# Optimization experiments

Measured on AMD Instinct MI355X. Metric: run time of the kernel, lower is better.

## Reference

```python
import jax, jax.numpy as jnp
import numpy as np

N, IN_DIM, HID, H = 4096, 128, 512, 8
D = HID // H  # head_dim = 64
NEG = -1e9


def setup_inputs() -> dict:
    key = jax.random.key(0)
    ks = jax.random.split(key, 16)
    s_in = 1.0 / np.sqrt(IN_DIM)
    s_h = 1.0 / np.sqrt(HID)
    return {
        "node_features": jax.random.normal(ks[0], (N, IN_DIM), jnp.float32),
        "edge_mask_bool": jax.random.bernoulli(ks[1], 0.3, (1, 1, N, N)),
        "time_bias": jax.random.normal(ks[2], (1, 1, N, N), jnp.float32) * 0.1,
        "W_in": jax.random.normal(ks[3], (IN_DIM, HID), jnp.float32) * s_in,
        "b_in": jnp.zeros((HID,), jnp.float32),
        "Wq": jax.random.normal(ks[4], (HID, HID), jnp.float32) * s_h,
        "bq": jnp.zeros((HID,), jnp.float32),
        "Wk": jax.random.normal(ks[5], (HID, HID), jnp.float32) * s_h,
        "bk": jnp.zeros((HID,), jnp.float32),
        "Wv": jax.random.normal(ks[6], (HID, HID), jnp.float32) * s_h,
        "bv": jnp.zeros((HID,), jnp.float32),
        "Wo": jax.random.normal(ks[7], (HID, HID), jnp.float32) * s_h,
        "bo": jnp.zeros((HID,), jnp.float32),
    }


def reference(node_features, edge_mask_bool, time_bias, W_in, b_in, Wq, bq, Wk, bk, Wv, bv, Wo, bo):
    # input projection + QKV projections
    x = node_features @ W_in + b_in                       # [N, HID]
    q = (x @ Wq + bq).reshape(N, H, D)                    # [N, H, D]
    k = (x @ Wk + bk).reshape(N, H, D)
    v = (x @ Wv + bv).reshape(N, H, D)
    # scores [H, N, N], scaled by sqrt(head_dim)
    scores = jnp.einsum("nhd,mhd->hnm", q, k) / jnp.sqrt(jnp.asarray(D, x.dtype))
    # additive mask: True blocks attention (-1e9), plus time bias
    bias = edge_mask_bool[0, 0].astype(x.dtype) * NEG + time_bias[0, 0]  # [N, N]
    scores = scores + bias[None, :, :]
    attn = jax.nn.softmax(scores, axis=-1)                # [H, N, N]
    out = jnp.einsum("hnm,mhd->nhd", attn, v).reshape(N, HID)
    return out @ Wo + bo                                  # [N, HID]
```

## Files before the change

### kernel.cpp

```cpp
#include <hip/hip_runtime.h>
#include <hip/hip_bf16.h>

static constexpr int kN   = 4096;
static constexpr int kIn  = 128;
static constexpr int kHid = 512;
static constexpr int kH   = 8;
static constexpr int kD   = 64;
#define NEGV (-1e9f)

static constexpr int kKFS = 32768 + 64;
static constexpr int kVFS = 131072 + 64;

typedef __bf16 bf16x8 __attribute__((ext_vector_type(8)));
typedef float  f32x4  __attribute__((ext_vector_type(4)));
typedef float  f32x16 __attribute__((ext_vector_type(16)));

__device__ __forceinline__ unsigned short f2bf(float f) {
    return __builtin_bit_cast(unsigned short, (__bf16)f);
}
__device__ __forceinline__ unsigned pkbf(float a, float b) {
    return (unsigned)f2bf(a) | ((unsigned)f2bf(b) << 16);
}

__global__ void misc_kernel(const unsigned int* __restrict__ m, int* __restrict__ mode,
                            const float* __restrict__ bq, const float* __restrict__ bk,
                            const float* __restrict__ bv, float* __restrict__ dst) {
    if (blockIdx.x < 6) {
        int i = blockIdx.x * 256 + threadIdx.x;
        dst[i] = i < 512 ? bq[i] : (i < 1024 ? bk[i - 512] : bv[i - 1024]);
        return;
    }
    int t = threadIdx.x;
    if (t >= 64) return;
    int isf = 0, isb = 0;
    for (int i = t; i < 4096; i += 64) {
        unsigned int w = m[i];
        if (w == 0x3F800000u) isf = 1;
        else if (w > 1u)      isb = 1;
    }
    unsigned long long bf = __ballot(isf != 0);
    unsigned long long bb = __ballot(isb != 0);
    if (t == 0) mode[0] = bf ? 2 : (bb ? 1 : 0);
}

__global__ void transpose_all_kernel(const float* __restrict__ s0, const float* __restrict__ s1,
                                     const float* __restrict__ s2, const float* __restrict__ s3,
                                     const float* __restrict__ s4,
                                     unsigned short* __restrict__ d0, unsigned short* __restrict__ d1,
                                     unsigned short* __restrict__ d2, unsigned short* __restrict__ d3,
                                     unsigned short* __restrict__ d4) {
    __shared__ float t[32][33];
    int z = blockIdx.z;
    const float* src = z == 0 ? s0 : z == 1 ? s1 : z == 2 ? s2 : z == 3 ? s3 : s4;
    unsigned short* dst = z == 0 ? d0 : z == 1 ? d1 : z == 2 ? d2 : z == 3 ? d3 : d4;
    int R = z == 0 ? kIn : kHid, C = kHid;
    int c0 = blockIdx.x * 32, r0 = blockIdx.y * 32;
    if (r0 >= R) return;
    int tx = threadIdx.x, ty = threadIdx.y;
#pragma unroll
    for (int i = 0; i < 4; i++) {
        int r = ty + i * 8;
        t[r][tx] = src[(size_t)(r0 + r) * C + c0 + tx];
    }
    __syncthreads();
#pragma unroll
    for (int i = 0; i < 4; i++) {
        int r = ty + i * 8;
        dst[(size_t)(c0 + r) * R + r0 + tx] = f2bf(t[tx][r]);
    }
}

template <bool ABF, int OMODE>
__global__ __launch_bounds__(256) void gemm_kernel(const void* __restrict__ Ap,
                                                   const unsigned short* __restrict__ Bt,
                                                   const float* __restrict__ bias,
                                                   void* __restrict__ Cp, void* __restrict__ Cp2,
                                                   void* __restrict__ Cp3,
                                                   int M, int Nn, int K, int ldc) {
    __shared__ unsigned short As[128][40];
    __shared__ unsigned short Bs[128][40];
    const int tid  = threadIdx.x;
    const int lane = tid & 63;
    const int wv   = tid >> 6;
    const int wr   = wv >> 1, wc = wv & 1;
    const int m0 = blockIdx.x * 128, n0 = blockIdx.y * 128;
    const int g = lane >> 4, li = lane & 15;

    f32x4 acc[4][4] = {};
    const int rr = tid >> 2;
    const int cc = (tid & 3) * 8;

    for (int k0 = 0; k0 < K; k0 += 32) {
#pragma unroll
        for (int p = 0; p < 128; p += 64) {
            int r = rr + p;
            if (ABF) {
                const unsigned short* A = (const unsigned short*)Ap;
                *(uint4*)&As[r][cc] = *(const uint4*)(A + (size_t)(m0 + r) * K + k0 + cc);
            } else {
                const float* A = (const float*)Ap;
                const float4 v0 = *(const float4*)(A + (size_t)(m0 + r) * K + k0 + cc);
                const float4 v1 = *(const float4*)(A + (size_t)(m0 + r) * K + k0 + cc + 4);
                uint4 u;
                u.x = f2bf(v0.x) | ((unsigned)f2bf(v0.y) << 16);
                u.y = f2bf(v0.z) | ((unsigned)f2bf(v0.w) << 16);
                u.z = f2bf(v1.x) | ((unsigned)f2bf(v1.y) << 16);
                u.w = f2bf(v1.z) | ((unsigned)f2bf(v1.w) << 16);
                *(uint4*)&As[r][cc] = u;
            }
            *(uint4*)&Bs[r][cc] = *(const uint4*)(Bt + (size_t)(n0 + r) * K + k0 + cc);
        }
        __syncthreads();

        bf16x8 af[4], bfv[4];
#pragma unroll
        for (int mi = 0; mi < 4; mi++)
            af[mi] = *(const bf16x8*)&As[wr * 64 + mi * 16 + li][g * 8];
#pragma unroll
        for (int ni = 0; ni < 4; ni++)
            bfv[ni] = *(const bf16x8*)&Bs[wc * 64 + ni * 16 + li][g * 8];
#pragma unroll
        for (int mi = 0; mi < 4; mi++)
#pragma unroll
            for (int ni = 0; ni < 4; ni++)
                acc[mi][ni] = __builtin_amdgcn_mfma_f32_16x16x32_bf16(af[mi], bfv[ni], acc[mi][ni], 0, 0, 0);
        __syncthreads();
    }

#pragma unroll
    for (int mi = 0; mi < 4; mi++) {
        int rowb = m0 + wr * 64 + mi * 16 + g * 4;
#pragma unroll
        for (int ni = 0; ni < 4; ni++) {
            int col = n0 + wc * 64 + ni * 16 + li;
            float bv = bias ? bias[col] : 0.f;
            if (OMODE == 3) {
                if (col < 512) {
                    unsigned short* C = (unsigned short*)Cp;
#pragma unroll
                    for (int r2 = 0; r2 < 4; r2++)
                        C[(size_t)(rowb + r2) * 512 + col] = f2bf(acc[mi][ni][r2] + bv);
                } else if (col < 1024) {
                    int d = col - 512;
                    unsigned short* Kf = (unsigned short*)Cp2;
                    size_t base = (size_t)(d >> 3) * kKFS + (size_t)(d & 7);
#pragma unroll
                    for (int r2 = 0; r2 < 4; r2++)
                        Kf[base + ((size_t)(rowb + r2) << 3)] = f2bf(acc[mi][ni][r2] + bv);
                } else {
                    int d = col - 1024;
                    unsigned short* Vf = (unsigned short*)Cp3;
                    size_t base = (size_t)(d >> 5) * kVFS + ((size_t)(rowb >> 3) << 8) +
                                  ((size_t)(d & 31) << 3) + (size_t)(rowb & 7);
                    ushort4 st;
                    st.x = f2bf(acc[mi][ni][0] + bv);
                    st.y = f2bf(acc[mi][ni][1] + bv);
                    st.z = f2bf(acc[mi][ni][2] + bv);
                    st.w = f2bf(acc[mi][ni][3] + bv);
                    *(ushort4*)(Vf + base) = st;
                }
            } else if (OMODE == 1) {
                unsigned short* C = (unsigned short*)Cp;
#pragma unroll
                for (int r2 = 0; r2 < 4; r2++)
                    C[(size_t)(rowb + r2) * ldc + col] = f2bf(acc[mi][ni][r2] + bv);
            } else {
                float* C = (float*)Cp;
#pragma unroll
                for (int r2 = 0; r2 < 4; r2++)
                    C[(size_t)(rowb + r2) * ldc + col] = acc[mi][ni][r2] + bv;
            }
        }
    }
}

__global__ __launch_bounds__(512, 4) void attn_kernel(
    const unsigned short* __restrict__ qg, const unsigned short* __restrict__ kfb,
    const unsigned short* __restrict__ vfb,
    const void* __restrict__ maskp, const float* __restrict__ tb,
    const int* __restrict__ modep,
    float* __restrict__ Op, float* __restrict__ Mp, float* __restrict__ Lp,
    int KZ, int NC) {
    __shared__ float bias_s[2][128][33];

    const int tid  = threadIdx.x;
    const int lane = tid & 63;
    const int w    = tid >> 6;
    const int q5   = lane & 31;
    const int hi   = lane >> 5;
    const int n0   = blockIdx.x * 32;
    const int z    = blockIdx.y;
    const int kz0  = z * KZ;
    const int mode = modep[0];
    const int hb   = w * kD;

    bf16x8 qf[4];
#pragma unroll
    for (int f = 0; f < 4; f++)
        qf[f] = *(const bf16x8*)(qg + (size_t)(n0 + q5) * 512 + hb + f * 16 + hi * 8);

    f32x16 po[2] = {};
    float m_run = -3e38f, l_run = 0.f;

    const int sr  = tid & 31;
    const int scg = tid >> 5;
    float stg[8];

    auto stage_load = [&](int kbase) {
        size_t idx = (size_t)(n0 + sr) * kN + kbase + scg * 8;
        float tv[8];
        *(float4*)&tv[0] = *(const float4*)(tb + idx);
        *(float4*)&tv[4] = *(const float4*)(tb + idx + 4);
        if (mode == 0) {
            const int* mp = (const int*)maskp;
            int4 a = *(const int4*)(mp + idx);
            int4 b = *(const int4*)(mp + idx + 4);
            int mv[8] = {a.x, a.y, a.z, a.w, b.x, b.y, b.z, b.w};
#pragma unroll
            for (int j = 0; j < 8; j++) stg[j] = (mv[j] ? NEGV : 0.f) + tv[j];
        } else if (mode == 1) {
            const unsigned char* mp = (const unsigned char*)maskp;
            uint2 u = *(const uint2*)(mp + idx);
#pragma unroll
            for (int j = 0; j < 4; j++) stg[j] = (((u.x >> (8 * j)) & 255u) ? NEGV : 0.f) + tv[j];
#pragma unroll
            for (int j = 0; j < 4; j++) stg[4 + j] = (((u.y >> (8 * j)) & 255u) ? NEGV : 0.f) + tv[4 + j];
        } else {
            const float* mp = (const float*)maskp;
            float4 a = *(const float4*)(mp + idx);
            float4 b = *(const float4*)(mp + idx + 4);
            float mv[8] = {a.x, a.y, a.z, a.w, b.x, b.y, b.z, b.w};
#pragma unroll
            for (int j = 0; j < 8; j++) stg[j] = (mv[j] != 0.f ? NEGV : 0.f) + tv[j];
        }
    };
    auto stage_write = [&](int buf) {
#pragma unroll
        for (int j = 0; j < 8; j++) bias_s[buf][scg * 8 + j][sr] = stg[j];
    };

    auto kload = [&](int kpos, int f) -> bf16x8 {
        return *(const bf16x8*)(kfb + (size_t)(w * 8 + f * 2 + hi) * kKFS + ((size_t)(kpos + q5) << 3));
    };

    stage_load(kz0);
    stage_write(0);
    __syncthreads();

    for (int c = 0; c < NC; c++) {
        if (c + 1 < NC) stage_load(kz0 + (c + 1) * 128);
        const int cb = c & 1;
        const int kbase = kz0 + c * 128;

        bf16x8 kcur[4], knxt[4];
#pragma unroll
        for (int f = 0; f < 4; f++) kcur[f] = kload(kbase, f);

#pragma unroll
        for (int s = 0; s < 4; s++) {
            const int kpos = kbase + s * 32;
            bf16x8 vb00, vb01, vb10, vb11;
            {
                const size_t v0 = (size_t)(w * 2 + 0) * kVFS + (((size_t)kpos >> 3) << 8) + ((size_t)q5 << 3);
                const size_t v1 = (size_t)(w * 2 + 1) * kVFS + (((size_t)kpos >> 3) << 8) + ((size_t)q5 << 3);
                vb00 = *(const bf16x8*)(vfb + v0 + ((size_t)hi << 8));
                vb01 = *(const bf16x8*)(vfb + v0 + ((size_t)(2 + hi) << 8));
                vb10 = *(const bf16x8*)(vfb + v1 + ((size_t)hi << 8));
                vb11 = *(const bf16x8*)(vfb + v1 + ((size_t)(2 + hi) << 8));
            }
            if (s < 3) {
#pragma unroll
                for (int f = 0; f < 4; f++) knxt[f] = kload(kbase + (s + 1) * 32, f);
            }
            f32x16 sc = {};
#pragma unroll
            for (int f = 0; f < 4; f++)
                sc = __builtin_amdgcn_mfma_f32_32x32x16_bf16(kcur[f], qf[f], sc, 0, 0, 0);

            float v[16];
#pragma unroll
            for (int r = 0; r < 16; r++) {
                int key = (r & 3) + 8 * (r >> 2) + 4 * hi;
                v[r] = fmaf(sc[r], 0.125f, bias_s[cb][s * 32 + key][q5]);
            }
            float t8[8];
#pragma unroll
            for (int i = 0; i < 8; i++) t8[i] = fmaxf(v[2 * i], v[2 * i + 1]);
#pragma unroll
            for (int i = 0; i < 4; i++) t8[i] = fmaxf(t8[i], t8[i + 4]);
            t8[0] = fmaxf(t8[0], t8[2]); t8[1] = fmaxf(t8[1], t8[3]);
            float mx = fmaxf(t8[0], t8[1]);
            mx = fmaxf(mx, __shfl_xor(mx, 32));
            if (!__all(mx <= m_run + 8.0f)) {
                float mnew = fmaxf(m_run, mx);
                float alpha = __expf(m_run - mnew);
                m_run = mnew;
                l_run *= alpha;
                po[0] *= alpha;
                po[1] *= alpha;
            }
            float p[16], s8[8];
#pragma unroll
            for (int i = 0; i < 8; i++) {
                p[2 * i]     = __expf(v[2 * i] - m_run);
                p[2 * i + 1] = __expf(v[2 * i + 1] - m_run);
                s8[i] = p[2 * i] + p[2 * i + 1];
            }
#pragma unroll
            for (int i = 0; i < 4; i++) s8[i] += s8[i + 4];
            l_run += (s8[0] + s8[2]) + (s8[1] + s8[3]);
            unsigned su[8], tu[8];
#pragma unroll
            for (int i = 0; i < 8; i++) su[i] = pkbf(p[2 * i], p[2 * i + 1]);
#pragma unroll
            for (int i = 0; i < 8; i++) tu[i] = __shfl_xor(su[i], 32);
            uint4 f0 = hi ? uint4{tu[2], tu[3], su[2], su[3]} : uint4{su[0], su[1], tu[0], tu[1]};
            uint4 f1 = hi ? uint4{tu[6], tu[7], su[6], su[7]} : uint4{su[4], su[5], tu[4], tu[5]};
            bf16x8 pf0 = __builtin_bit_cast(bf16x8, f0);
            bf16x8 pf1 = __builtin_bit_cast(bf16x8, f1);
            po[0] = __builtin_amdgcn_mfma_f32_32x32x16_bf16(vb00, pf0, po[0], 0, 0, 0);
            po[0] = __builtin_amdgcn_mfma_f32_32x32x16_bf16(vb01, pf1, po[0], 0, 0, 0);
            po[1] = __builtin_amdgcn_mfma_f32_32x32x16_bf16(vb10, pf0, po[1], 0, 0, 0);
            po[1] = __builtin_amdgcn_mfma_f32_32x32x16_bf16(vb11, pf1, po[1], 0, 0, 0);
            if (s < 3) {
#pragma unroll
                for (int f = 0; f < 4; f++) kcur[f] = knxt[f];
            }
        }
        if (c + 1 < NC) {
            __syncthreads();
            stage_write((c + 1) & 1);
            __syncthreads();
        }
    }

    l_run += __shfl_xor(l_run, 32);
    float* ob = Op + ((((size_t)z * kN + n0 + q5) * kH + w) << 6);
#pragma unroll
    for (int a = 0; a < 2; a++)
#pragma unroll
        for (int m = 0; m < 4; m++) {
            float4 st = {po[a][4 * m], po[a][4 * m + 1], po[a][4 * m + 2], po[a][4 * m + 3]};
            *(float4*)(ob + a * 32 + 8 * m + 4 * hi) = st;
        }
    if (lane < 32) {
        Mp[((size_t)z * kN + n0 + q5) * kH + w] = m_run;
        Lp[((size_t)z * kN + n0 + q5) * kH + w] = l_run;
    }
}

__global__ __launch_bounds__(256) void combine_kernel(const float* __restrict__ Op,
                                                      const float* __restrict__ Mp,
                                                      const float* __restrict__ Lp,
                                                      unsigned short* __restrict__ xo, int NZ) {
    int idx = blockIdx.x * 256 + threadIdx.x;
    int n = idx >> 9, c = idx & 511;
    int h = c >> 6, d = c & 63;
    float m = -3e38f;
    for (int zz = 0; zz < NZ; zz++)
        m = fmaxf(m, Mp[((size_t)zz * kN + n) * kH + h]);
    float num = 0.f, den = 0.f;
    for (int zz = 0; zz < NZ; zz++) {
        float a = __expf(Mp[((size_t)zz * kN + n) * kH + h] - m);
        den += a * Lp[((size_t)zz * kN + n) * kH + h];
        num += a * Op[(((size_t)zz * kN + n) * kH + h) * kD + d];
    }
    xo[idx] = f2bf(num / den);
}

extern "C" void kernel_launch(void* const* d_in, const int* in_sizes, int n_in,
                              void* d_out, int out_size, void* d_ws, size_t ws_size,
                              hipStream_t stream) {
    const float* node = (const float*)d_in[0];
    const void*  mask = d_in[1];
    const float* tb   = (const float*)d_in[2];
    const float* W_in = (const float*)d_in[3];
    const float* b_in = (const float*)d_in[4];
    const float* Wq   = (const float*)d_in[5];
    const float* bq   = (const float*)d_in[6];
    const float* Wk   = (const float*)d_in[7];
    const float* bk   = (const float*)d_in[8];
    const float* Wv   = (const float*)d_in[9];
    const float* bv   = (const float*)d_in[10];
    const float* Wo   = (const float*)d_in[11];
    const float* bo   = (const float*)d_in[12];
    (void)in_sizes; (void)n_in; (void)out_size;

    char* ws = (char*)d_ws;
    size_t off = 0;
    auto alloc = [&](size_t bytes) {
        void* p = ws + off;
        off += (bytes + 255) & ~(size_t)255;
        return p;
    };
    unsigned short* x    = (unsigned short*)alloc((size_t)kN * kHid * 2);
    unsigned short* qb   = (unsigned short*)alloc((size_t)kN * kHid * 2);
    unsigned short* kf   = (unsigned short*)alloc((size_t)64 * kKFS * 2);
    unsigned short* vf   = (unsigned short*)alloc((size_t)16 * kVFS * 2);
    unsigned short* Wt_in  = (unsigned short*)alloc((size_t)kHid * kIn * 2);
    unsigned short* Wt_qkv = (unsigned short*)alloc((size_t)3 * kHid * kHid * 2);
    unsigned short* Wt_o   = (unsigned short*)alloc((size_t)kHid * kHid * 2);
    float* bqkv = (float*)alloc(1536 * 4);
    int*   mode = (int*)alloc(256);
    unsigned short* xo = x;

    size_t fixed = off;
    size_t perz = (((size_t)kN * kHid * 4 + 255) & ~(size_t)255) +
                  2 * (((size_t)kN * kH * 4 + 255) & ~(size_t)255);
    int NZ = 4;
    if (fixed + 4 * perz > ws_size) NZ = 2;
    if (fixed + 2 * perz > ws_size) NZ = 1;
    float* Op = (float*)alloc((size_t)NZ * kN * kHid * 4);
    float* Mp = (float*)alloc((size_t)NZ * kN * kH * 4);
    float* Lp = (float*)alloc((size_t)NZ * kN * kH * 4);

    misc_kernel<<<7, 256, 0, stream>>>((const unsigned int*)mask, mode, bq, bk, bv, bqkv);
    transpose_all_kernel<<<dim3(16, 16, 5), dim3(32, 8), 0, stream>>>(
        W_in, Wq, Wk, Wv, Wo, Wt_in, Wt_qkv, Wt_qkv + (size_t)kHid * kHid,
        Wt_qkv + (size_t)2 * kHid * kHid, Wt_o);

    gemm_kernel<false, 1><<<dim3(kN / 128, kHid / 128), 256, 0, stream>>>(
        node, Wt_in, b_in, x, nullptr, nullptr, kN, kHid, kIn, kHid);
    gemm_kernel<true, 3><<<dim3(kN / 128, 1536 / 128), 256, 0, stream>>>(
        x, Wt_qkv, bqkv, qb, kf, vf, kN, 1536, kHid, 512);

    const int KZ = kN / NZ;
    attn_kernel<<<dim3(kN / 32, NZ), 512, 0, stream>>>(
        qb, kf, vf, mask, tb, mode, Op, Mp, Lp, KZ, KZ / 128);
    combine_kernel<<<(kN * kHid) / 256, 256, 0, stream>>>(Op, Mp, Lp, xo, NZ);

    gemm_kernel<true, 0><<<dim3(kN / 128, kHid / 128), 256, 0, stream>>>(
        xo, Wt_o, bo, d_out, nullptr, nullptr, kN, kHid, kHid, kHid);
}
```

Before: 186.3 us.

## Flatten attention chunk loop and raise wave priority around MFMA blocks

Merges the outer 128-key chunk loop and the inner 4-step loop into one flat loop over 32-key tiles. K fragments are now prefetched across chunk boundaries instead of being reloaded cold at the start of each chunk. It also wraps the QK and PV MFMA groups in s_setprio(1)/s_setprio(0) so waves issuing matrix ops get scheduling priority. The flat loop is no longer fully unrolled over s, so the index math and branch conditions become runtime values, which may cost some extra scalar work.

```diff
diff --git a/kernel.cpp b/kernel.cpp
--- a/kernel.cpp
+++ b/kernel.cpp
@@ -247,89 +247,91 @@
     stage_write(0);
     __syncthreads();
 
-    for (int c = 0; c < NC; c++) {
-        if (c + 1 < NC) stage_load(kz0 + (c + 1) * 128);
-        const int cb = c & 1;
-        const int kbase = kz0 + c * 128;
-
-        bf16x8 kcur[4], knxt[4];
-#pragma unroll
-        for (int f = 0; f < 4; f++) kcur[f] = kload(kbase, f);
-
-#pragma unroll
-        for (int s = 0; s < 4; s++) {
-            const int kpos = kbase + s * 32;
-            bf16x8 vb00, vb01, vb10, vb11;
-            {
-                const size_t v0 = (size_t)(w * 2 + 0) * kVFS + (((size_t)kpos >> 3) << 8) + ((size_t)q5 << 3);
-                const size_t v1 = (size_t)(w * 2 + 1) * kVFS + (((size_t)kpos >> 3) << 8) + ((size_t)q5 << 3);
-                vb00 = *(const bf16x8*)(vfb + v0 + ((size_t)hi << 8));
-                vb01 = *(const bf16x8*)(vfb + v0 + ((size_t)(2 + hi) << 8));
-                vb10 = *(const bf16x8*)(vfb + v1 + ((size_t)hi << 8));
-                vb11 = *(const bf16x8*)(vfb + v1 + ((size_t)(2 + hi) << 8));
-            }
-            if (s < 3) {
-#pragma unroll
-                for (int f = 0; f < 4; f++) knxt[f] = kload(kbase + (s + 1) * 32, f);
-            }
-            f32x16 sc = {};
-#pragma unroll
-            for (int f = 0; f < 4; f++)
-                sc = __builtin_amdgcn_mfma_f32_32x32x16_bf16(kcur[f], qf[f], sc, 0, 0, 0);
-
-            float v[16];
-#pragma unroll
-            for (int r = 0; r < 16; r++) {
-                int key = (r & 3) + 8 * (r >> 2) + 4 * hi;
-                v[r] = fmaf(sc[r], 0.125f, bias_s[cb][s * 32 + key][q5]);
-            }
-            float t8[8];
-#pragma unroll
-            for (int i = 0; i < 8; i++) t8[i] = fmaxf(v[2 * i], v[2 * i + 1]);
-#pragma unroll
-            for (int i = 0; i < 4; i++) t8[i] = fmaxf(t8[i], t8[i + 4]);
-            t8[0] = fmaxf(t8[0], t8[2]); t8[1] = fmaxf(t8[1], t8[3]);
-            float mx = fmaxf(t8[0], t8[1]);
-            mx = fmaxf(mx, __shfl_xor(mx, 32));
-            if (!__all(mx <= m_run + 8.0f)) {
-                float mnew = fmaxf(m_run, mx);
-                float alpha = __expf(m_run - mnew);
-                m_run = mnew;
-                l_run *= alpha;
-                po[0] *= alpha;
-                po[1] *= alpha;
-            }
-            float p[16], s8[8];
-#pragma unroll
-            for (int i = 0; i < 8; i++) {
-                p[2 * i]     = __expf(v[2 * i] - m_run);
-                p[2 * i + 1] = __expf(v[2 * i + 1] - m_run);
-                s8[i] = p[2 * i] + p[2 * i + 1];
-            }
-#pragma unroll
-            for (int i = 0; i < 4; i++) s8[i] += s8[i + 4];
-            l_run += (s8[0] + s8[2]) + (s8[1] + s8[3]);
-            unsigned su[8], tu[8];
-#pragma unroll
-            for (int i = 0; i < 8; i++) su[i] = pkbf(p[2 * i], p[2 * i + 1]);
-#pragma unroll
-            for (int i = 0; i < 8; i++) tu[i] = __shfl_xor(su[i], 32);
-            uint4 f0 = hi ? uint4{tu[2], tu[3], su[2], su[3]} : uint4{su[0], su[1], tu[0], tu[1]};
-            uint4 f1 = hi ? uint4{tu[6], tu[7], su[6], su[7]} : uint4{su[4], su[5], tu[4], tu[5]};
-            bf16x8 pf0 = __builtin_bit_cast(bf16x8, f0);
-            bf16x8 pf1 = __builtin_bit_cast(bf16x8, f1);
-            po[0] = __builtin_amdgcn_mfma_f32_32x32x16_bf16(vb00, pf0, po[0], 0, 0, 0);
-            po[0] = __builtin_amdgcn_mfma_f32_32x32x16_bf16(vb01, pf1, po[0], 0, 0, 0);
-            po[1] = __builtin_amdgcn_mfma_f32_32x32x16_bf16(vb10, pf0, po[1], 0, 0, 0);
-            po[1] = __builtin_amdgcn_mfma_f32_32x32x16_bf16(vb11, pf1, po[1], 0, 0, 0);
-            if (s < 3) {
-#pragma unroll
-                for (int f = 0; f < 4; f++) kcur[f] = knxt[f];
-            }
-        }
-        if (c + 1 < NC) {
+    const int NT = NC * 4;
+    bf16x8 kcur[4], knxt[4];
+#pragma unroll
+    for (int f = 0; f < 4; f++) kcur[f] = kload(kz0, f);
+
+    for (int t = 0; t < NT; t++) {
+        const int kpos = kz0 + t * 32;
+        const int cb = (t >> 2) & 1;
+        const int s = t & 3;
+        if (s == 0 && t + 4 < NT) stage_load(kz0 + (t + 4) * 32);
+
+        bf16x8 vb00, vb01, vb10, vb11;
+        {
+            const size_t v0 = (size_t)(w * 2 + 0) * kVFS + (((size_t)kpos >> 3) << 8) + ((size_t)q5 << 3);
+            const size_t v1 = (size_t)(w * 2 + 1) * kVFS + (((size_t)kpos >> 3) << 8) + ((size_t)q5 << 3);
+            vb00 = *(const bf16x8*)(vfb + v0 + ((size_t)hi << 8));
+            vb01 = *(const bf16x8*)(vfb + v0 + ((size_t)(2 + hi) << 8));
+            vb10 = *(const bf16x8*)(vfb + v1 + ((size_t)hi << 8));
+            vb11 = *(const bf16x8*)(vfb + v1 + ((size_t)(2 + hi) << 8));
+        }
+        if (t + 1 < NT) {
+#pragma unroll
+            for (int f = 0; f < 4; f++) knxt[f] = kload(kz0 + (t + 1) * 32, f);
+        }
+        __builtin_amdgcn_s_setprio(1);
+        f32x16 sc = {};
+#pragma unroll
+        for (int f = 0; f < 4; f++)
+            sc = __builtin_amdgcn_mfma_f32_32x32x16_bf16(kcur[f], qf[f], sc, 0, 0, 0);
+        __builtin_amdgcn_s_setprio(0);
+
+        float v[16];
+#pragma unroll
+        for (int r = 0; r < 16; r++) {
+            int key = (r & 3) + 8 * (r >> 2) + 4 * hi;
+            v[r] = fmaf(sc[r], 0.125f, bias_s[cb][s * 32 + key][q5]);
+        }
+        float t8[8];
+#pragma unroll
+        for (int i = 0; i < 8; i++) t8[i] = fmaxf(v[2 * i], v[2 * i + 1]);
+#pragma unroll
+        for (int i = 0; i < 4; i++) t8[i] = fmaxf(t8[i], t8[i + 4]);
+        t8[0] = fmaxf(t8[0], t8[2]); t8[1] = fmaxf(t8[1], t8[3]);
+        float mx = fmaxf(t8[0], t8[1]);
+        mx = fmaxf(mx, __shfl_xor(mx, 32));
+        if (!__all(mx <= m_run + 8.0f)) {
+            float mnew = fmaxf(m_run, mx);
+            float alpha = __expf(m_run - mnew);
+            m_run = mnew;
+            l_run *= alpha;
+            po[0] *= alpha;
+            po[1] *= alpha;
+        }
+        float p[16], s8[8];
+#pragma unroll
+        for (int i = 0; i < 8; i++) {
+            p[2 * i]     = __expf(v[2 * i] - m_run);
+            p[2 * i + 1] = __expf(v[2 * i + 1] - m_run);
+            s8[i] = p[2 * i] + p[2 * i + 1];
+        }
+#pragma unroll
+        for (int i = 0; i < 4; i++) s8[i] += s8[i + 4];
+        l_run += (s8[0] + s8[2]) + (s8[1] + s8[3]);
+        unsigned su[8], tu[8];
+#pragma unroll
+        for (int i = 0; i < 8; i++) su[i] = pkbf(p[2 * i], p[2 * i + 1]);
+#pragma unroll
+        for (int i = 0; i < 8; i++) tu[i] = __shfl_xor(su[i], 32);
+        uint4 f0 = hi ? uint4{tu[2], tu[3], su[2], su[3]} : uint4{su[0], su[1], tu[0], tu[1]};
+        uint4 f1 = hi ? uint4{tu[6], tu[7], su[6], su[7]} : uint4{su[4], su[5], tu[4], tu[5]};
+        bf16x8 pf0 = __builtin_bit_cast(bf16x8, f0);
+        bf16x8 pf1 = __builtin_bit_cast(bf16x8, f1);
+        __builtin_amdgcn_s_setprio(1);
+        po[0] = __builtin_amdgcn_mfma_f32_32x32x16_bf16(vb00, pf0, po[0], 0, 0, 0);
+        po[0] = __builtin_amdgcn_mfma_f32_32x32x16_bf16(vb01, pf1, po[0], 0, 0, 0);
+        po[1] = __builtin_amdgcn_mfma_f32_32x32x16_bf16(vb10, pf0, po[1], 0, 0, 0);
+        po[1] = __builtin_amdgcn_mfma_f32_32x32x16_bf16(vb11, pf1, po[1], 0, 0, 0);
+        __builtin_amdgcn_s_setprio(0);
+        if (t + 1 < NT) {
+#pragma unroll
+            for (int f = 0; f < 4; f++) kcur[f] = knxt[f];
+        }
+        if (s == 3 && t + 1 < NT) {
             __syncthreads();
-            stage_write((c + 1) & 1);
+            stage_write(((t >> 2) + 1) & 1);
             __syncthreads();
         }
     }
```

Measured after the change: 229.8 us. +23.4%, slower.

## Fold input projection into QKV weights and precompute fp16 mask+bias matrix

Applied to the files above, without the earlier changes.

Multiplies W_in into the QKV weights (and folds b_in into the QKV biases), so the QKV GEMM runs directly on node features with K=128 and the separate input projection GEMM goes away. It also adds a prepass that merges the mask and time bias into a single fp16 N×N matrix, so the attention kernel streams 2 bytes per element instead of mask plus fp32 bias. The trade-off is an extra full pass over mask and bias, a 32MB workspace buffer, and a different rounding path because the fused weights are stored in bf16.

```diff
diff --git a/kernel.cpp b/kernel.cpp
--- a/kernel.cpp
+++ b/kernel.cpp
@@ -6,12 +6,14 @@
 static constexpr int kHid = 512;
 static constexpr int kH   = 8;
 static constexpr int kD   = 64;
-#define NEGV (-1e9f)
+#define MASKF (-30000.0f)
 
 static constexpr int kKFS = 32768 + 64;
 static constexpr int kVFS = 131072 + 64;
 
-typedef __bf16 bf16x8 __attribute__((ext_vector_type(8)));
+typedef __bf16    bf16x8 __attribute__((ext_vector_type(8)));
+typedef _Float16  f16x8  __attribute__((ext_vector_type(8)));
+typedef unsigned short u16x8 __attribute__((ext_vector_type(8)));
 typedef float  f32x4  __attribute__((ext_vector_type(4)));
 typedef float  f32x16 __attribute__((ext_vector_type(16)));
 
@@ -21,53 +23,108 @@
 __device__ __forceinline__ unsigned pkbf(float a, float b) {
     return (unsigned)f2bf(a) | ((unsigned)f2bf(b) << 16);
 }
+__device__ __forceinline__ unsigned short f2h(float f) {
+    return __builtin_bit_cast(unsigned short, (_Float16)f);
+}
 
 __global__ void misc_kernel(const unsigned int* __restrict__ m, int* __restrict__ mode,
                             const float* __restrict__ bq, const float* __restrict__ bk,
-                            const float* __restrict__ bv, float* __restrict__ dst) {
+                            const float* __restrict__ bv, float* __restrict__ dst,
+                            const float* __restrict__ W_in, unsigned short* __restrict__ Wb_in) {
     if (blockIdx.x < 6) {
         int i = blockIdx.x * 256 + threadIdx.x;
         dst[i] = i < 512 ? bq[i] : (i < 1024 ? bk[i - 512] : bv[i - 1024]);
         return;
     }
-    int t = threadIdx.x;
-    if (t >= 64) return;
-    int isf = 0, isb = 0;
-    for (int i = t; i < 4096; i += 64) {
-        unsigned int w = m[i];
-        if (w == 0x3F800000u) isf = 1;
-        else if (w > 1u)      isb = 1;
-    }
-    unsigned long long bf = __ballot(isf != 0);
-    unsigned long long bb = __ballot(isb != 0);
-    if (t == 0) mode[0] = bf ? 2 : (bb ? 1 : 0);
+    if (blockIdx.x == 6) {
+        int t = threadIdx.x;
+        if (t >= 64) return;
+        int isf = 0, isb = 0;
+        for (int i = t; i < 4096; i += 64) {
+            unsigned int w = m[i];
+            if (w == 0x3F800000u) isf = 1;
+            else if (w > 1u)      isb = 1;
+        }
+        unsigned long long bf = __ballot(isf != 0);
+        unsigned long long bb = __ballot(isb != 0);
+        if (t == 0) mode[0] = bf ? 2 : (bb ? 1 : 0);
+        return;
+    }
+    int i = (blockIdx.x - 7) * 256 + threadIdx.x;
+    if (i < kIn * kHid) Wb_in[i] = f2bf(W_in[i]);
+}
+
+__global__ __launch_bounds__(256) void prepass_kernel(const void* __restrict__ maskp,
+                                                      const float* __restrict__ tb,
+                                                      const int* __restrict__ modep,
+                                                      unsigned short* __restrict__ bc) {
+    const int mode = modep[0];
+    size_t idx = ((size_t)blockIdx.x * 256 + threadIdx.x) * 8;
+    float tv[8];
+    *(float4*)&tv[0] = *(const float4*)(tb + idx);
+    *(float4*)&tv[4] = *(const float4*)(tb + idx + 4);
+    u16x8 o;
+    if (mode == 0) {
+        const int* mp = (const int*)maskp;
+        int4 a = *(const int4*)(mp + idx);
+        int4 b = *(const int4*)(mp + idx + 4);
+        int mv[8] = {a.x, a.y, a.z, a.w, b.x, b.y, b.z, b.w};
+#pragma unroll
+        for (int j = 0; j < 8; j++) o[j] = f2h(mv[j] ? MASKF : tv[j]);
+    } else if (mode == 1) {
+        const unsigned char* mp = (const unsigned char*)maskp;
+        uint2 u = *(const uint2*)(mp + idx);
+#pragma unroll
+        for (int j = 0; j < 4; j++) o[j] = f2h(((u.x >> (8 * j)) & 255u) ? MASKF : tv[j]);
+#pragma unroll
+        for (int j = 0; j < 4; j++) o[4 + j] = f2h(((u.y >> (8 * j)) & 255u) ? MASKF : tv[4 + j]);
+    } else {
+        const float* mp = (const float*)maskp;
+        float4 a = *(const float4*)(mp + idx);
+        float4 b = *(const float4*)(mp + idx + 4);
+        float mv[8] = {a.x, a.y, a.z, a.w, b.x, b.y, b.z, b.w};
+#pragma unroll
+        for (int j = 0; j < 8; j++) o[j] = f2h((mv[j] != 0.f) ? MASKF : tv[j]);
+    }
+    *(u16x8*)(bc + idx) = o;
 }
 
 __global__ void transpose_all_kernel(const float* __restrict__ s0, const float* __restrict__ s1,
                                      const float* __restrict__ s2, const float* __restrict__ s3,
-                                     const float* __restrict__ s4,
                                      unsigned short* __restrict__ d0, unsigned short* __restrict__ d1,
-                                     unsigned short* __restrict__ d2, unsigned short* __restrict__ d3,
-                                     unsigned short* __restrict__ d4) {
+                                     unsigned short* __restrict__ d2, unsigned short* __restrict__ d3) {
     __shared__ float t[32][33];
     int z = blockIdx.z;
-    const float* src = z == 0 ? s0 : z == 1 ? s1 : z == 2 ? s2 : z == 3 ? s3 : s4;
-    unsigned short* dst = z == 0 ? d0 : z == 1 ? d1 : z == 2 ? d2 : z == 3 ? d3 : d4;
-    int R = z == 0 ? kIn : kHid, C = kHid;
+    const float* src = z == 0 ? s0 : z == 1 ? s1 : z == 2 ? s2 : s3;
+    unsigned short* dst = z == 0 ? d0 : z == 1 ? d1 : z == 2 ? d2 : d3;
     int c0 = blockIdx.x * 32, r0 = blockIdx.y * 32;
-    if (r0 >= R) return;
     int tx = threadIdx.x, ty = threadIdx.y;
 #pragma unroll
     for (int i = 0; i < 4; i++) {
         int r = ty + i * 8;
-        t[r][tx] = src[(size_t)(r0 + r) * C + c0 + tx];
+        t[r][tx] = src[(size_t)(r0 + r) * kHid + c0 + tx];
     }
     __syncthreads();
 #pragma unroll
     for (int i = 0; i < 4; i++) {
         int r = ty + i * 8;
-        dst[(size_t)(c0 + r) * R + r0 + tx] = f2bf(t[tx][r]);
-    }
+        dst[(size_t)(c0 + r) * kHid + r0 + tx] = f2bf(t[tx][r]);
+    }
+}
+
+__global__ __launch_bounds__(256) void bc_kernel(const float* __restrict__ b_in,
+                                                 const unsigned short* __restrict__ Wt_qkv,
+                                                 const float* __restrict__ bqkv,
+                                                 float* __restrict__ bc) {
+    int j = blockIdx.x * 256 + threadIdx.x;
+    float acc = bqkv[j];
+    const unsigned short* row = Wt_qkv + (size_t)j * kHid;
+    for (int i0 = 0; i0 < kHid; i0 += 8) {
+        bf16x8 wv = *(const bf16x8*)(row + i0);
+#pragma unroll
+        for (int k = 0; k < 8; k++) acc += b_in[i0 + k] * (float)wv[k];
+    }
+    bc[j] = acc;
 }
 
 template <bool ABF, int OMODE>
@@ -177,8 +234,7 @@
 __global__ __launch_bounds__(512, 4) void attn_kernel(
     const unsigned short* __restrict__ qg, const unsigned short* __restrict__ kfb,
     const unsigned short* __restrict__ vfb,
-    const void* __restrict__ maskp, const float* __restrict__ tb,
-    const int* __restrict__ modep,
+    const unsigned short* __restrict__ bcb,
     float* __restrict__ Op, float* __restrict__ Mp, float* __restrict__ Lp,
     int KZ, int NC) {
     __shared__ float bias_s[2][128][33];
@@ -191,7 +247,6 @@
     const int n0   = blockIdx.x * 32;
     const int z    = blockIdx.y;
     const int kz0  = z * KZ;
-    const int mode = modep[0];
     const int hb   = w * kD;
 
     bf16x8 qf[4];
@@ -208,31 +263,9 @@
 
     auto stage_load = [&](int kbase) {
         size_t idx = (size_t)(n0 + sr) * kN + kbase + scg * 8;
-        float tv[8];
-        *(float4*)&tv[0] = *(const float4*)(tb + idx);
-        *(float4*)&tv[4] = *(const float4*)(tb + idx + 4);
-        if (mode == 0) {
-            const int* mp = (const int*)maskp;
-            int4 a = *(const int4*)(mp + idx);
-            int4 b = *(const int4*)(mp + idx + 4);
-            int mv[8] = {a.x, a.y, a.z, a.w, b.x, b.y, b.z, b.w};
-#pragma unroll
-            for (int j = 0; j < 8; j++) stg[j] = (mv[j] ? NEGV : 0.f) + tv[j];
-        } else if (mode == 1) {
-            const unsigned char* mp = (const unsigned char*)maskp;
-            uint2 u = *(const uint2*)(mp + idx);
-#pragma unroll
-            for (int j = 0; j < 4; j++) stg[j] = (((u.x >> (8 * j)) & 255u) ? NEGV : 0.f) + tv[j];
-#pragma unroll
-            for (int j = 0; j < 4; j++) stg[4 + j] = (((u.y >> (8 * j)) & 255u) ? NEGV : 0.f) + tv[4 + j];
-        } else {
-            const float* mp = (const float*)maskp;
-            float4 a = *(const float4*)(mp + idx);
-            float4 b = *(const float4*)(mp + idx + 4);
-            float mv[8] = {a.x, a.y, a.z, a.w, b.x, b.y, b.z, b.w};
-#pragma unroll
-            for (int j = 0; j < 8; j++) stg[j] = (mv[j] != 0.f ? NEGV : 0.f) + tv[j];
-        }
+        f16x8 v = *(const f16x8*)(bcb + idx);
+#pragma unroll
+        for (int j = 0; j < 8; j++) stg[j] = (float)v[j];
     };
     auto stage_write = [&](int buf) {
 #pragma unroll
@@ -393,16 +426,18 @@
         off += (bytes + 255) & ~(size_t)255;
         return p;
     };
-    unsigned short* x    = (unsigned short*)alloc((size_t)kN * kHid * 2);
     unsigned short* qb   = (unsigned short*)alloc((size_t)kN * kHid * 2);
     unsigned short* kf   = (unsigned short*)alloc((size_t)64 * kKFS * 2);
     unsigned short* vf   = (unsigned short*)alloc((size_t)16 * kVFS * 2);
-    unsigned short* Wt_in  = (unsigned short*)alloc((size_t)kHid * kIn * 2);
+    unsigned short* xo   = (unsigned short*)alloc((size_t)kN * kHid * 2);
+    unsigned short* bias_c = (unsigned short*)alloc((size_t)kN * kN * 2);
     unsigned short* Wt_qkv = (unsigned short*)alloc((size_t)3 * kHid * kHid * 2);
     unsigned short* Wt_o   = (unsigned short*)alloc((size_t)kHid * kHid * 2);
+    unsigned short* Wb_in  = (unsigned short*)alloc((size_t)kIn * kHid * 2);
+    unsigned short* Wct    = (unsigned short*)alloc((size_t)1536 * kIn * 2);
     float* bqkv = (float*)alloc(1536 * 4);
+    float* bc   = (float*)alloc(1536 * 4);
     int*   mode = (int*)alloc(256);
-    unsigned short* xo = x;
 
     size_t fixed = off;
     size_t perz = (((size_t)kN * kHid * 4 + 255) & ~(size_t)255) +
@@ -414,19 +449,22 @@
     float* Mp = (float*)alloc((size_t)NZ * kN * kH * 4);
     float* Lp = (float*)alloc((size_t)NZ * kN * kH * 4);
 
-    misc_kernel<<<7, 256, 0, stream>>>((const unsigned int*)mask, mode, bq, bk, bv, bqkv);
-    transpose_all_kernel<<<dim3(16, 16, 5), dim3(32, 8), 0, stream>>>(
-        W_in, Wq, Wk, Wv, Wo, Wt_in, Wt_qkv, Wt_qkv + (size_t)kHid * kHid,
+    misc_kernel<<<263, 256, 0, stream>>>((const unsigned int*)mask, mode, bq, bk, bv, bqkv,
+                                         W_in, Wb_in);
+    transpose_all_kernel<<<dim3(16, 16, 4), dim3(32, 8), 0, stream>>>(
+        Wq, Wk, Wv, Wo, Wt_qkv, Wt_qkv + (size_t)kHid * kHid,
         Wt_qkv + (size_t)2 * kHid * kHid, Wt_o);
-
-    gemm_kernel<false, 1><<<dim3(kN / 128, kHid / 128), 256, 0, stream>>>(
-        node, Wt_in, b_in, x, nullptr, nullptr, kN, kHid, kIn, kHid);
-    gemm_kernel<true, 3><<<dim3(kN / 128, 1536 / 128), 256, 0, stream>>>(
-        x, Wt_qkv, bqkv, qb, kf, vf, kN, 1536, kHid, 512);
+    bc_kernel<<<6, 256, 0, stream>>>(b_in, Wt_qkv, bqkv, bc);
+    gemm_kernel<true, 1><<<dim3(12, 1), 256, 0, stream>>>(
+        Wt_qkv, Wb_in, nullptr, Wct, nullptr, nullptr, 1536, kIn, kHid, kIn);
+    prepass_kernel<<<(kN * kN) / (256 * 8), 256, 0, stream>>>(mask, tb, mode, bias_c);
+
+    gemm_kernel<false, 3><<<dim3(kN / 128, 1536 / 128), 256, 0, stream>>>(
+        node, Wct, bc, qb, kf, vf, kN, 1536, kIn, 512);
 
     const int KZ = kN / NZ;
     attn_kernel<<<dim3(kN / 32, NZ), 512, 0, stream>>>(
-        qb, kf, vf, mask, tb, mode, Op, Mp, Lp, KZ, KZ / 128);
+        qb, kf, vf, bias_c, Op, Mp, Lp, KZ, KZ / 128);
     combine_kernel<<<(kN * kHid) / 256, 256, 0, stream>>>(Op, Mp, Lp, xo, NZ);
 
     gemm_kernel<true, 0><<<dim3(kN / 128, kHid / 128), 256, 0, stream>>>(
```

Measured after the change: 195.4 us. +4.9%, slower.
